# Optimization experiments

Measured on AMD Instinct MI355X. Metric: run time of the kernel, lower is better.

Reference implementation:

```python
import jax, jax.numpy as jnp
import numpy as np
from jax import lax

EPS = 1e-5
C, H, W, G = 512, 32, 32, 32


def instance_norm(x):
    # torch InstanceNorm2d: affine=False, biased variance over (H,W)
    mu = x.mean(axis=(2, 3), keepdims=True)
    var = ((x - mu) ** 2).mean(axis=(2, 3), keepdims=True)
    return (x - mu) / jnp.sqrt(var + EPS)


def conv2d(x, w, stride=1, padding=0, groups=1, lhs_dilation=None):
    return lax.conv_general_dilated(
        x, w, (stride, stride), [(padding, padding)] * 2,
        lhs_dilation=lhs_dilation, feature_group_count=groups,
        dimension_numbers=('NCHW', 'OIHW', 'NCHW'))


def leaky_relu(x):
    return jnp.where(x >= 0, x, 0.2 * x)


def unfold(img, k, s):
    # img: (C,H,W) -> (nH*nW, C, k, k); matches torch unfold(1,k,s).unfold(2,k,s)
    c, h, w = img.shape
    nH = (h - k) // s + 1
    nW = (w - k) // s + 1
    rows = []
    for i in range(k):
        cols = [img[:, i:i + s * (nH - 1) + 1:s, j:j + s * (nW - 1) + 1:s] for j in range(k)]
        rows.append(jnp.stack(cols, axis=-1))  # (C,nH,nW,k)
    p = jnp.stack(rows, axis=-2)  # (C,nH,nW,k,k)
    return p.transpose(1, 2, 0, 3, 4).reshape(nH * nW, c, k, k)


def ral(bg, fg, rate=2, ksize=3, scale=10.0):
    # Region Affinity Layer (contextual-attention style), batch = 1
    b, c, h, w = fg.shape
    fh, fw = h // rate, w // rate
    # bilinear downsample by exactly 2 (half-pixel) == 2x2 average pooling
    fg_small = fg.reshape(b, c, fh, rate, fw, rate).mean(axis=(3, 5))
    bk = 2 * rate
    bg_patches = unfold(jnp.pad(bg, ((0, 0), (0, 0), (1, 1), (1, 1)))[0], bk, rate)      # (256,C,4,4)
    fg_patches = unfold(jnp.pad(fg_small, ((0, 0), (0, 0), (1, 1), (1, 1)))[0], ksize, 1)  # (256,C,3,3)
    norm = jnp.sqrt((fg_patches ** 2).sum(axis=(1, 2, 3), keepdims=True))
    fgp_n = fg_patches / jnp.maximum(norm, 1e-4)
    score = conv2d(fg_small, fgp_n, padding=1)        # (1,256,16,16)
    attn = jax.nn.softmax(score * scale, axis=1)
    # conv_transpose2d(attn, bg_patches, stride=rate, padding=1) via lhs dilation
    w_t = jnp.flip(bg_patches, axis=(-2, -1)).transpose(1, 0, 2, 3)  # (C,256,4,4)
    return conv2d(attn, w_t, padding=bk - 2, lhs_dilation=(rate, rate)) / 4.0  # (1,C,32,32)


def forward(x, gus, w_sk3, b_sk3, w_sk5, b_sk5, w_sk7, b_sk7,
            w_fc, b_fc, w_fc0, b_fc0, w_fc1, b_fc1, w_fc2, b_fc2, w_down, w_fuse):
    # ---- SKConv (M=3 branches: k=3/5/7, groups=32) ----
    feas = []
    for wgt, bias, pad in ((w_sk3, b_sk3, 1), (w_sk5, b_sk5, 2), (w_sk7, b_sk7, 3)):
        f = conv2d(x, wgt, padding=pad, groups=G) + bias[None, :, None, None]
        feas.append(jax.nn.relu(instance_norm(f)))
    feas = jnp.stack(feas, axis=1)                # (B,3,C,H,W)
    fea_s = feas.sum(axis=1).mean(axis=(2, 3))    # (B,C) global pool
    fea_z = fea_s @ w_fc.T + b_fc                 # (B,32)
    att = jnp.stack([fea_z @ w_fc0.T + b_fc0,
                     fea_z @ w_fc1.T + b_fc1,
                     fea_z @ w_fc2.T + b_fc2], axis=1)  # (B,3,C)
    att = jax.nn.softmax(att, axis=1)[..., None, None]
    out_32 = (feas * att).sum(axis=1)             # (1,C,32,32)
    out_res = out_32
    out_32 = ral(out_32, out_32)
    b, c, h, w = out_32.shape
    # ---- gaussian-weighted broadcast sum: (P,H,W)x(C,H,W)->(P,C)->raw reshape ----
    gus_out = jnp.einsum('pxy,cxy->pc', gus, out_32[0]).reshape(b, c, h, w)
    # ---- CSA patch correlation ----
    csa2_in = jax.nn.sigmoid(out_32)
    p_fff = unfold(jnp.pad(out_32, ((0, 0), (0, 0), (1, 1), (1, 1)))[0], 3, 1)    # (1024,C,3,3)
    p_f = unfold(jnp.pad(csa2_in, ((0, 0), (0, 0), (1, 1), (1, 1)))[0], 3, 1)     # (1024,C,3,3)
    p_conv = unfold(csa2_in[0], 1, 1)                                             # (1024,C,1,1)
    csa_a = (p_conv * p_f).mean(axis=1)                                           # (1024,3,3)
    csa_a = jax.nn.softmax(csa_a.reshape(h * w, 9), axis=1).reshape(h * w, 1, 3, 3)
    out_csa = (csa_a * p_fff).sum(axis=(-2, -1)).reshape(b, c, h, w)
    # ---- fuse ----
    z = jnp.concatenate([gus_out, out_csa], axis=1)       # (1,1024,32,32)
    z = leaky_relu(instance_norm(conv2d(z, w_down)))
    z = jnp.concatenate([z, out_res], axis=1)             # (1,1024,32,32)
    return leaky_relu(instance_norm(conv2d(z, w_fuse)))   # (1,512,32,32)


def _gaussian_buffer():
    # util.gussin(1.5): gaussian centered at every grid position of a 32x32 map
    v = 1.5
    r = np.arange(32)
    i, k, x, y = np.meshgrid(r, r, r, r, indexing='ij')
    g = np.exp(-((x - i) ** 2 + (y - k) ** 2) / (2 * v * v)) / (2 * np.pi * v * v)
    return jnp.asarray(g.reshape(32 * 32, 32, 32), dtype=jnp.float32)


def setup_inputs():
    key = jax.random.key(0)
    ks = jax.random.split(key, 12)
    s = 0.02
    return {
        'x': jax.random.normal(ks[0], (1, C, H, W), jnp.float32),
        'gus': _gaussian_buffer(),
        'w_sk3': jax.random.normal(ks[1], (C, C // G, 3, 3), jnp.float32) * s,
        'b_sk3': jnp.zeros((C,), jnp.float32),
        'w_sk5': jax.random.normal(ks[2], (C, C // G, 5, 5), jnp.float32) * s,
        'b_sk5': jnp.zeros((C,), jnp.float32),
        'w_sk7': jax.random.normal(ks[3], (C, C // G, 7, 7), jnp.float32) * s,
        'b_sk7': jnp.zeros((C,), jnp.float32),
        'w_fc': jax.random.normal(ks[4], (32, C), jnp.float32) * s,
        'b_fc': jnp.zeros((32,), jnp.float32),
        'w_fc0': jax.random.normal(ks[5], (C, 32), jnp.float32) * s,
        'b_fc0': jnp.zeros((C,), jnp.float32),
        'w_fc1': jax.random.normal(ks[6], (C, 32), jnp.float32) * s,
        'b_fc1': jnp.zeros((C,), jnp.float32),
        'w_fc2': jax.random.normal(ks[7], (C, 32), jnp.float32) * s,
        'b_fc2': jnp.zeros((C,), jnp.float32),
        'w_down': jax.random.normal(ks[8], (512, 1024, 1, 1), jnp.float32) * s,
        'w_fuse': jax.random.normal(ks[9], (512, 1024, 1, 1), jnp.float32) * s,
    }


def reference(x, gus, w_sk3, b_sk3, w_sk5, b_sk5, w_sk7, b_sk7, w_fc, b_fc,
              w_fc0, b_fc0, w_fc1, b_fc1, w_fc2, b_fc2, w_down, w_fuse):
    return forward(x, gus, w_sk3, b_sk3, w_sk5, b_sk5, w_sk7, b_sk7,
                   w_fc, b_fc, w_fc0, b_fc0, w_fc1, b_fc1, w_fc2, b_fc2,
                   w_down, w_fuse)
```

## Files before the change

### kernel.cpp

```cpp
#include <hip/hip_runtime.h>
#include <math.h>

#define EPSN 1e-5f

typedef __attribute__((ext_vector_type(8))) short bf16x8;
typedef __attribute__((ext_vector_type(4))) float f32x4;

__device__ __forceinline__ ushort f2bf(float f) {
  unsigned u = __float_as_uint(f);
  unsigned r = (u + 0x7fff + ((u >> 16) & 1)) >> 16;
  return (ushort)r;
}
__device__ __forceinline__ float bf2f(ushort h) {
  return __uint_as_float(((unsigned)h) << 16);
}

__device__ __forceinline__ void breduce2(float& a, float& b, float* lds) {
#pragma unroll
  for (int o = 32; o > 0; o >>= 1) {
    a += __shfl_down(a, o);
    b += __shfl_down(b, o);
  }
  int lane = threadIdx.x & 63, wid = threadIdx.x >> 6;
  __syncthreads();
  if (lane == 0) { lds[wid] = a; lds[4 + wid] = b; }
  __syncthreads();
  a = lds[0] + lds[1] + lds[2] + lds[3];
  b = lds[4] + lds[5] + lds[6] + lds[7];
}

__device__ __forceinline__ float breduce_sum(float v, float* lds) {
#pragma unroll
  for (int o = 32; o > 0; o >>= 1) v += __shfl_down(v, o);
  int lane = threadIdx.x & 63, wid = threadIdx.x >> 6;
  __syncthreads();
  if (lane == 0) lds[wid] = v;
  __syncthreads();
  return lds[0] + lds[1] + lds[2] + lds[3];
}

__device__ __forceinline__ float breduce_max(float v, float* lds) {
#pragma unroll
  for (int o = 32; o > 0; o >>= 1) v = fmaxf(v, __shfl_down(v, o));
  int lane = threadIdx.x & 63, wid = threadIdx.x >> 6;
  __syncthreads();
  if (lane == 0) lds[wid] = v;
  __syncthreads();
  return fmaxf(fmaxf(lds[0], lds[1]), fmaxf(lds[2], lds[3]));
}

__global__ void pre_kernel(const float* __restrict__ gus,
                           const float* __restrict__ wdown,
                           const float* __restrict__ wfuse,
                           const float* __restrict__ w3,
                           const float* __restrict__ w5,
                           const float* __restrict__ w7,
                           ushort* __restrict__ gus_bf,
                           ushort* __restrict__ wdown_bf,
                           ushort* __restrict__ wfuse_bf,
                           ushort* __restrict__ resd,
                           ushort* __restrict__ Apk_g) {
  int bid = blockIdx.x, tid = threadIdx.x;
  if (bid < 2048) {
    int i = bid * 1024 + tid * 4;
    const float* src; ushort* dst; int off;
    if (i < 1048576) { src = gus; dst = gus_bf; off = i; }
    else if (i < 1572864) { src = wdown; dst = wdown_bf; off = i - 1048576; }
    else { src = wfuse; dst = wfuse_bf; off = i - 1572864; }
    float4 v = *(const float4*)&src[off];
    ushort4 o = {f2bf(v.x), f2bf(v.y), f2bf(v.z), f2bf(v.w)};
    *(ushort4*)&dst[off] = o;
  } else if (bid < 2304) {
    int t8 = (bid - 2048) * 256 + tid;
    uint4 z = {0u, 0u, 0u, 0u};
#pragma unroll
    for (int k = 0; k < 4; ++k) *(uint4*)&resd[(size_t)(t8 + k * 65536) * 8] = z;
  } else {
    int i2 = (bid - 2304) * 256 + tid;
    int g = i2 / 22016;
    int r = i2 - g * 22016;
    int p = r >> 9;
    int r5 = r & 511;
    int quad = r5 >> 7, m16 = (r5 >> 3) & 15, j = r & 7;
    int k = quad * 8 + j, tp = k >> 4, ic = k & 15;
    float val = 0.f;
    if (p < 25) {
      int t = 2 * p + tp;
      if (t < 49) val = w7[(size_t)(g * 16 + m16) * 784 + ic * 49 + t];
    } else if (p < 38) {
      int t = 2 * (p - 25) + tp;
      if (t < 25) val = w5[(size_t)(g * 16 + m16) * 400 + ic * 25 + t];
    } else {
      int t = 2 * (p - 38) + tp;
      if (t < 9) val = w3[(size_t)(g * 16 + m16) * 144 + ic * 9 + t];
    }
    Apk_g[i2] = f2bf(val);
  }
}

__global__ __launch_bounds__(256) void sk_mfma(const float* __restrict__ x,
                                               const ushort* __restrict__ Apk_g,
                                               ushort* __restrict__ feasRawH) {
  __shared__ ushort xg[10 * 38 * 24];
  int bid = blockIdx.x, tid = threadIdx.x;
  int g = bid >> 3, sl = bid & 7, y0 = sl * 4;
  for (int i = tid; i < 4560; i += 256) ((uint*)xg)[i] = 0u;
  __syncthreads();
  for (int i = tid; i < 5120; i += 256) {
    int lr = i >> 9, ic = (i >> 5) & 15, xc = i & 31;
    int y = y0 + lr - 3;
    if ((unsigned)y < 32u)
      xg[(lr * 38 + xc + 3) * 24 + ic] =
          f2bf(x[(size_t)(g * 16 + ic) * 1024 + y * 32 + xc]);
  }
  __syncthreads();
  int wv = tid >> 6, lane = tid & 63, quad = lane >> 4, m16 = lane & 15;
  int qh = (quad & 1) * 8, tp = quad >> 1;
  const ushort* Ag = Apk_g + (size_t)g * 22016;
  f32x4 acc[2][3] = {};
  for (int p = 0; p < 25; ++p) {
    bf16x8 af = *(const bf16x8*)&Ag[(p * 4 + quad) * 128 + m16 * 8];
    int t = 2 * p + tp;
    if (t > 48) t = 48;
    int ky = t / 7, kx = t - ky * 7;
#pragma unroll
    for (int ti = 0; ti < 2; ++ti) {
      int T = wv + ti * 4, tl = T >> 1, x0c = (T & 1) * 16;
      bf16x8 bf = *(const bf16x8*)&xg[((tl + ky) * 38 + x0c + m16 + kx) * 24 + qh];
      acc[ti][2] = __builtin_amdgcn_mfma_f32_16x16x32_bf16(af, bf, acc[ti][2], 0, 0, 0);
    }
  }
  for (int p = 0; p < 13; ++p) {
    bf16x8 af = *(const bf16x8*)&Ag[((p + 25) * 4 + quad) * 128 + m16 * 8];
    int t = 2 * p + tp;
    if (t > 24) t = 24;
    int ky = t / 5, kx = t - ky * 5;
#pragma unroll
    for (int ti = 0; ti < 2; ++ti) {
      int T = wv + ti * 4, tl = T >> 1, x0c = (T & 1) * 16;
      bf16x8 bf =
          *(const bf16x8*)&xg[((tl + ky + 1) * 38 + x0c + m16 + kx + 1) * 24 + qh];
      acc[ti][1] = __builtin_amdgcn_mfma_f32_16x16x32_bf16(af, bf, acc[ti][1], 0, 0, 0);
    }
  }
  for (int p = 0; p < 5; ++p) {
    bf16x8 af = *(const bf16x8*)&Ag[((p + 38) * 4 + quad) * 128 + m16 * 8];
    int t = 2 * p + tp;
    if (t > 8) t = 8;
    int ky = t / 3, kx = t - ky * 3;
#pragma unroll
    for (int ti = 0; ti < 2; ++ti) {
      int T = wv + ti * 4, tl = T >> 1, x0c = (T & 1) * 16;
      bf16x8 bf =
          *(const bf16x8*)&xg[((tl + ky + 2) * 38 + x0c + m16 + kx + 2) * 24 + qh];
      acc[ti][0] = __builtin_amdgcn_mfma_f32_16x16x32_bf16(af, bf, acc[ti][0], 0, 0, 0);
    }
  }
  int cb = g * 16 + quad * 4;
#pragma unroll
  for (int ti = 0; ti < 2; ++ti) {
    int T = wv + ti * 4, tl = T >> 1, x0c = (T & 1) * 16;
    int pos = (y0 + tl) * 32 + x0c + m16;
#pragma unroll
    for (int br = 0; br < 3; ++br)
#pragma unroll
      for (int r = 0; r < 4; ++r)
        feasRawH[(size_t)(br * 512 + cb + r) * 1024 + pos] = f2bf(acc[ti][br][r]);
  }
}

__global__ __launch_bounds__(256) void sk_norm(const ushort* __restrict__ rawH,
                                               ushort* __restrict__ feasH,
                                               float* __restrict__ bmean) {
  __shared__ float red[8];
  int mc = blockIdx.x, tid = threadIdx.x;
  float v[4];
  {
    ushort4 h = *(const ushort4*)&rawH[(size_t)mc * 1024 + tid * 4];
    v[0] = bf2f(h.x); v[1] = bf2f(h.y); v[2] = bf2f(h.z); v[3] = bf2f(h.w);
  }
  float s = 0.f, ss = 0.f;
#pragma unroll
  for (int r = 0; r < 4; ++r) { s += v[r]; ss += v[r] * v[r]; }
  breduce2(s, ss, red);
  float mean = s * (1.f / 1024.f);
  float var = ss * (1.f / 1024.f) - mean * mean;
  float inv = rsqrtf(var + EPSN);
  float rs = 0.f;
  ushort4 o;
#pragma unroll
  for (int r = 0; r < 4; ++r) {
    float t = (v[r] - mean) * inv;
    t = t > 0.f ? t : 0.f;
    ((ushort*)&o)[r] = f2bf(t);
    rs += t;
  }
  *(ushort4*)&feasH[(size_t)mc * 1024 + tid * 4] = o;
  float tot = breduce_sum(rs, red);
  if (tid == 0) bmean[mc] = tot * (1.f / 1024.f);
}

__global__ __launch_bounds__(256) void blend_fc(
    const ushort* __restrict__ feasH, const float* __restrict__ bmean,
    const float* __restrict__ wfc, const float* __restrict__ bfc,
    const float* __restrict__ w0, const float* __restrict__ b0,
    const float* __restrict__ w1, const float* __restrict__ b1,
    const float* __restrict__ w2, const float* __restrict__ b2,
    float* __restrict__ res, ushort* __restrict__ Zt2,
    ushort* __restrict__ resd) {
  __shared__ float sfea[512];
  __shared__ float zpart[8][32];
  __shared__ float zz[32];
  __shared__ float lv[3][32];
  __shared__ float attb[3][32];
  __shared__ float tile[32][33];
  int tid = threadIdx.x;
  int pb = blockIdx.x * 32, cb = blockIdx.y * 32;
  for (int c = tid; c < 512; c += 256)
    sfea[c] = bmean[c] + bmean[512 + c] + bmean[1024 + c];
  __syncthreads();
  {
    int j = tid & 31, seg = tid >> 5;
    float p = 0.f;
    for (int c = seg * 64; c < seg * 64 + 64; ++c) p += sfea[c] * wfc[j * 512 + c];
    zpart[seg][j] = p;
  }
  __syncthreads();
  if (tid < 32) {
    float d = bfc[tid];
#pragma unroll
    for (int s = 0; s < 8; ++s) d += zpart[s][tid];
    zz[tid] = d;
  }
  __syncthreads();
  if (tid < 96) {
    int m = tid >> 5, cl = tid & 31;
    const float* wm = (m == 0) ? w0 : (m == 1) ? w1 : w2;
    const float* bm = (m == 0) ? b0 : (m == 1) ? b1 : b2;
    float l = bm[cb + cl];
#pragma unroll
    for (int j = 0; j < 32; ++j) l += zz[j] * wm[(cb + cl) * 32 + j];
    lv[m][cl] = l;
  }
  __syncthreads();
  if (tid < 32) {
    float l0 = lv[0][tid], l1 = lv[1][tid], l2 = lv[2][tid];
    float mx = fmaxf(l0, fmaxf(l1, l2));
    float e0 = expf(l0 - mx), e1 = expf(l1 - mx), e2 = expf(l2 - mx);
    float inv = 1.f / (e0 + e1 + e2);
    attb[0][tid] = e0 * inv; attb[1][tid] = e1 * inv; attb[2][tid] = e2 * inv;
  }
  __syncthreads();
  int tx = tid & 31, ty = tid >> 5;
  int pos = pb + tx;
  int yy = pos >> 5, xx = pos & 31;
  int ki0 = (yy + 1) & 1, pi0 = (yy + 1 - ki0) >> 1;
  int kj0 = (xx + 1) & 1, pj0 = (xx + 1 - kj0) >> 1;
#pragma unroll
  for (int r = 0; r < 4; ++r) {
    int cl = ty + r * 8;
    int c = cb + cl;
    float v = bf2f(feasH[(size_t)c * 1024 + pos]) * attb[0][cl] +
              bf2f(feasH[(size_t)(512 + c) * 1024 + pos]) * attb[1][cl] +
              bf2f(feasH[(size_t)(1024 + c) * 1024 + pos]) * attb[2][cl];
    res[c * 1024 + pos] = v;
    tile[cl][tx] = v;
    ushort bv16 = f2bf(v);
#pragma unroll
    for (int ai = 0; ai < 2; ++ai) {
      int ki = ki0 + 2 * ai, pi = pi0 - ai;
      if ((unsigned)pi >= 16u) continue;
#pragma unroll
      for (int aj = 0; aj < 2; ++aj) {
        int kj = kj0 + 2 * aj, pj = pj0 - aj;
        if ((unsigned)pj >= 16u) continue;
        resd[((size_t)(ki * 4 + kj) << 17) + (size_t)c * 256 + pi * 16 + pj] = bv16;
      }
    }
  }
  __syncthreads();
#pragma unroll
  for (int r = 0; r < 4; ++r) {
    int pl = ty + r * 8;
    Zt2[(size_t)(pb + pl) * 1024 + 512 + cb + tx] = f2bf(tile[tx][pl]);
  }
}

__global__ __launch_bounds__(256) void gram_part2(const float* __restrict__ res,
                                                  float* __restrict__ Apart) {
  __shared__ float ch[4][324];
  int tid = threadIdx.x;
  int qb = blockIdx.x * 64, pb = blockIdx.y * 64;
  int kc = blockIdx.z;
  int tx = tid & 15, ty = tid >> 4;
  for (int i = tid; i < 4 * 324; i += 256) ((float*)ch)[i] = 0.f;
  int pi = (pb + ty * 4) >> 4, pj = (pb + ty * 4) & 15;
  int qi = (qb + tx * 4) >> 4, qj = (qb + tx * 4) & 15;
  int lane = tid & 63, wv = tid >> 6;
  int sr = lane >> 2, sc = (lane & 3) * 4;
  float acc[4][4] = {};
  for (int c0 = kc * 16; c0 < kc * 16 + 16; c0 += 4) {
    __syncthreads();
    {
      const float* src = res + (size_t)(c0 + wv) * 1024 + (2 * sr) * 32 + 2 * sc;
      float4 r0a = *(const float4*)src;
      float4 r0b = *(const float4*)(src + 4);
      float4 r1a = *(const float4*)(src + 32);
      float4 r1b = *(const float4*)(src + 36);
      float* dst = &ch[wv][(sr + 1) * 18 + sc + 1];
      dst[0] = 0.25f * (r0a.x + r0a.y + r1a.x + r1a.y);
      dst[1] = 0.25f * (r0a.z + r0a.w + r1a.z + r1a.w);
      dst[2] = 0.25f * (r0b.x + r0b.y + r1b.x + r1b.y);
      dst[3] = 0.25f * (r0b.z + r0b.w + r1b.z + r1b.w);
    }
    __syncthreads();
#pragma unroll
    for (int cc = 0; cc < 4; ++cc) {
      float ps[3][6], qs[3][6];
#pragma unroll
      for (int u = 0; u < 3; ++u) {
        const float* pr = &ch[cc][(pi + u) * 18 + pj];
        const float* qr = &ch[cc][(qi + u) * 18 + qj];
#pragma unroll
        for (int t = 0; t < 6; ++t) { ps[u][t] = pr[t]; qs[u][t] = qr[t]; }
      }
#pragma unroll
      for (int u = 0; u < 3; ++u)
#pragma unroll
        for (int v = 0; v < 3; ++v)
#pragma unroll
          for (int i = 0; i < 4; ++i)
#pragma unroll
            for (int j = 0; j < 4; ++j)
              acc[i][j] += ps[u][v + i] * qs[u][v + j];
    }
  }
#pragma unroll
  for (int i = 0; i < 4; ++i) {
    float4 o4 = {acc[i][0], acc[i][1], acc[i][2], acc[i][3]};
    *(float4*)&Apart[(size_t)kc * 65536 + (pb + ty * 4 + i) * 256 + qb + tx * 4] = o4;
  }
}

__global__ __launch_bounds__(256) void attn_soft3(const float* __restrict__ Apart,
                                                  ushort* __restrict__ attnT) {
  __shared__ float red[8];
  int q = blockIdx.x, t = threadIdx.x;
  float d = 0.f, s = 0.f;
#pragma unroll
  for (int k = 0; k < 32; ++k) {
    d += Apart[(size_t)k * 65536 + t * 257];
    s += Apart[(size_t)k * 65536 + q * 256 + t];
  }
  float invn = 10.f / fmaxf(sqrtf(fmaxf(d, 0.f)), 1e-4f);
  float v = s * invn;
  float mx = breduce_max(v, red);
  float e = expf(v - mx);
  float sm = breduce_sum(e, red);
  attnT[q * 256 + t] = f2bf(e / sm);
}

__global__ __launch_bounds__(256) void mfma_tconv(const ushort* __restrict__ attnT,
                                                  const ushort* __restrict__ resd,
                                                  float* __restrict__ T) {
  int tid = threadIdx.x;
  int wv = tid >> 6, lane = tid & 63;
  int quad = lane >> 4, m16 = lane & 15;
  int nb = blockIdx.x * 64, qb = blockIdx.y * 64;
  int b = blockIdx.z;
  const ushort* Ap = attnT + (size_t)(qb + wv * 16 + m16) * 256 + quad * 8;
  const ushort* Bp = resd + (size_t)b * 131072 + (size_t)(nb + m16) * 256 + quad * 8;
  f32x4 ac0 = {0.f, 0.f, 0.f, 0.f}, ac1 = ac0, ac2 = ac0, ac3 = ac0;
#pragma unroll 2
  for (int k0 = 0; k0 < 256; k0 += 32) {
    bf16x8 af = *(const bf16x8*)(Ap + k0);
    bf16x8 b0 = *(const bf16x8*)(Bp + k0);
    bf16x8 b1 = *(const bf16x8*)(Bp + 16 * 256 + k0);
    bf16x8 b2 = *(const bf16x8*)(Bp + 32 * 256 + k0);
    bf16x8 b3 = *(const bf16x8*)(Bp + 48 * 256 + k0);
    ac0 = __builtin_amdgcn_mfma_f32_16x16x32_bf16(af, b0, ac0, 0, 0, 0);
    ac1 = __builtin_amdgcn_mfma_f32_16x16x32_bf16(af, b1, ac1, 0, 0, 0);
    ac2 = __builtin_amdgcn_mfma_f32_16x16x32_bf16(af, b2, ac2, 0, 0, 0);
    ac3 = __builtin_amdgcn_mfma_f32_16x16x32_bf16(af, b3, ac3, 0, 0, 0);
  }
  int row = qb + wv * 16 + quad * 4;
  float* Cb = T + (size_t)b * 131072;
  f32x4 accs[4] = {ac0, ac1, ac2, ac3};
#pragma unroll
  for (int nt = 0; nt < 4; ++nt)
#pragma unroll
    for (int r = 0; r < 4; ++r)
      Cb[(size_t)(row + r) * 512 + nb + nt * 16 + m16] = accs[nt][r];
}

__global__ __launch_bounds__(256) void tcomb2(const float* __restrict__ T,
                                              float* __restrict__ orlt,
                                              float* __restrict__ sigt,
                                              ushort* __restrict__ orlT) {
  __shared__ float tl[32][33];
  int nb = blockIdx.x * 32, cb = blockIdx.y * 32;
  int tx = threadIdx.x & 31, ty = threadIdx.x >> 5;
#pragma unroll
  for (int r = 0; r < 4; ++r) {
    int nl = ty + r * 8;
    int n = nb + nl, c = cb + tx;
    int y = n >> 5, x = n & 31;
    int i0 = (y + 1) >> 1, ki0 = (y + 1) & 1;
    int j0 = (x + 1) >> 1, kj0 = (x + 1) & 1;
    float sum = 0.f;
#pragma unroll
    for (int iy = 0; iy < 2; ++iy) {
      int i = i0 - iy, ki = ki0 + 2 * iy;
      if ((unsigned)i >= 16u) continue;
#pragma unroll
      for (int ix = 0; ix < 2; ++ix) {
        int j = j0 - ix, kj = kj0 + 2 * ix;
        if ((unsigned)j >= 16u) continue;
        sum += T[((ki * 4 + kj) * 256 + i * 16 + j) * 512 + c];
      }
    }
    float v = sum * 0.25f;
    orlt[n * 512 + c] = v;
    sigt[n * 512 + c] = 1.f / (1.f + expf(-v));
    tl[nl][tx] = v;
  }
  __syncthreads();
#pragma unroll
  for (int r = 0; r < 4; ++r) {
    int cl = ty + r * 8;
    orlT[(size_t)(cb + cl) * 1024 + nb + tx] = f2bf(tl[tx][cl]);
  }
}

__global__ __launch_bounds__(256) void gus_csa(
    const ushort* __restrict__ gus_bf, const ushort* __restrict__ orlT,
    const float* __restrict__ sigt, const float* __restrict__ orlt,
    ushort* __restrict__ Zt) {
  __shared__ float red9[4][9];
  __shared__ float a9s[9];
  int tid = threadIdx.x;
  if (blockIdx.x < 128) {
    const int K = 1024;
    int wv = tid >> 6, lane = tid & 63;
    int quad = lane >> 4, m16 = lane & 15;
    int nb = (blockIdx.x & 7) * 64, mb = (blockIdx.x >> 3) * 64;
    const ushort* Ap = gus_bf + (size_t)(mb + wv * 16 + m16) * K + quad * 8;
    const ushort* Bp = orlT + (size_t)(nb + m16) * K + quad * 8;
    f32x4 ac0 = {0.f, 0.f, 0.f, 0.f}, ac1 = ac0, ac2 = ac0, ac3 = ac0;
#pragma unroll 2
    for (int k0 = 0; k0 < K; k0 += 32) {
      bf16x8 af = *(const bf16x8*)(Ap + k0);
      bf16x8 b0 = *(const bf16x8*)(Bp + k0);
      bf16x8 b1 = *(const bf16x8*)(Bp + (size_t)16 * K + k0);
      bf16x8 b2 = *(const bf16x8*)(Bp + (size_t)32 * K + k0);
      bf16x8 b3 = *(const bf16x8*)(Bp + (size_t)48 * K + k0);
      ac0 = __builtin_amdgcn_mfma_f32_16x16x32_bf16(af, b0, ac0, 0, 0, 0);
      ac1 = __builtin_amdgcn_mfma_f32_16x16x32_bf16(af, b1, ac1, 0, 0, 0);
      ac2 = __builtin_amdgcn_mfma_f32_16x16x32_bf16(af, b2, ac2, 0, 0, 0);
      ac3 = __builtin_amdgcn_mfma_f32_16x16x32_bf16(af, b3, ac3, 0, 0, 0);
    }
    int row = mb + wv * 16 + quad * 4;
    f32x4 accs[4] = {ac0, ac1, ac2, ac3};
#pragma unroll
    for (int nt = 0; nt < 4; ++nt) {
      int c = nb + nt * 16 + m16;
#pragma unroll
      for (int r = 0; r < 4; ++r) {
        int p = row + r;
        int pos = ((p & 1) << 9) + c;
        int kk = p >> 1;
        Zt[(size_t)pos * 1024 + kk] = f2bf(accs[nt][r]);
      }
    }
    return;
  }
  int n = blockIdx.x - 128;
  int ny = n >> 5, nx = n & 31;
  int c2 = tid * 2;
  int lane = tid & 63, wid = tid >> 6;
  float2 ctr = *(const float2*)&sigt[n * 512 + c2];
  float part[9];
#pragma unroll
  for (int u = 0; u < 3; ++u) {
    int yy = ny + u - 1;
#pragma unroll
    for (int v = 0; v < 3; ++v) {
      int xx = nx + v - 1;
      float2 nb2 = {0.f, 0.f};
      if ((unsigned)yy < 32u && (unsigned)xx < 32u)
        nb2 = *(const float2*)&sigt[(yy * 32 + xx) * 512 + c2];
      part[u * 3 + v] = ctr.x * nb2.x + ctr.y * nb2.y;
    }
  }
#pragma unroll
  for (int t = 0; t < 9; ++t)
#pragma unroll
    for (int o = 32; o > 0; o >>= 1) part[t] += __shfl_down(part[t], o);
  if (lane == 0)
#pragma unroll
    for (int t = 0; t < 9; ++t) red9[wid][t] = part[t];
  __syncthreads();
  if (tid == 0) {
    float a[9];
#pragma unroll
    for (int t = 0; t < 9; ++t)
      a[t] = (red9[0][t] + red9[1][t] + red9[2][t] + red9[3][t]) * (1.f / 512.f);
    float mx = a[0];
#pragma unroll
    for (int t = 1; t < 9; ++t) mx = fmaxf(mx, a[t]);
    float sum = 0.f;
#pragma unroll
    for (int t = 0; t < 9; ++t) { a[t] = expf(a[t] - mx); sum += a[t]; }
    float inv = 1.f / sum;
#pragma unroll
    for (int t = 0; t < 9; ++t) a9s[t] = a[t] * inv;
  }
  __syncthreads();
  float2 acc = {0.f, 0.f};
#pragma unroll
  for (int u = 0; u < 3; ++u) {
    int yy = ny + u - 1;
#pragma unroll
    for (int v = 0; v < 3; ++v) {
      int xx = nx + v - 1;
      if ((unsigned)yy < 32u && (unsigned)xx < 32u) {
        float w = a9s[u * 3 + v];
        float2 ov = *(const float2*)&orlt[(yy * 32 + xx) * 512 + c2];
        acc.x += w * ov.x;
        acc.y += w * ov.y;
      }
    }
  }
  int kk = 512 + (n >> 1);
  int pos0 = ((n & 1) << 9) + c2;
  Zt[(size_t)pos0 * 1024 + kk] = f2bf(acc.x);
  Zt[(size_t)(pos0 + 1) * 1024 + kk] = f2bf(acc.y);
}

__global__ __launch_bounds__(256) void mfma_gemm_ks(const ushort* __restrict__ A,
                                                    const ushort* __restrict__ Bt,
                                                    float* __restrict__ Cp,
                                                    int N) {
  const int KF = 1024;
  int tid = threadIdx.x;
  int wv = tid >> 6, lane = tid & 63;
  int quad = lane >> 4, m16 = lane & 15;
  int nb = blockIdx.x * 64, mb = blockIdx.y * 64;
  int kh = blockIdx.z;
  const ushort* Ap = A + (size_t)(mb + wv * 16 + m16) * KF + kh * 512 + quad * 8;
  const ushort* Bp = Bt + (size_t)(nb + m16) * KF + kh * 512 + quad * 8;
  f32x4 ac0 = {0.f, 0.f, 0.f, 0.f}, ac1 = ac0, ac2 = ac0, ac3 = ac0;
#pragma unroll 2
  for (int k0 = 0; k0 < 512; k0 += 32) {
    bf16x8 af = *(const bf16x8*)(Ap + k0);
    bf16x8 b0 = *(const bf16x8*)(Bp + k0);
    bf16x8 b1 = *(const bf16x8*)(Bp + (size_t)16 * KF + k0);
    bf16x8 b2 = *(const bf16x8*)(Bp + (size_t)32 * KF + k0);
    bf16x8 b3 = *(const bf16x8*)(Bp + (size_t)48 * KF + k0);
    ac0 = __builtin_amdgcn_mfma_f32_16x16x32_bf16(af, b0, ac0, 0, 0, 0);
    ac1 = __builtin_amdgcn_mfma_f32_16x16x32_bf16(af, b1, ac1, 0, 0, 0);
    ac2 = __builtin_amdgcn_mfma_f32_16x16x32_bf16(af, b2, ac2, 0, 0, 0);
    ac3 = __builtin_amdgcn_mfma_f32_16x16x32_bf16(af, b3, ac3, 0, 0, 0);
  }
  int row = mb + wv * 16 + quad * 4;
  float* C = Cp + (size_t)kh * 524288;
  f32x4 accs[4] = {ac0, ac1, ac2, ac3};
#pragma unroll
  for (int nt = 0; nt < 4; ++nt)
#pragma unroll
    for (int r = 0; r < 4; ++r)
      C[(size_t)(row + r) * N + nb + nt * 16 + m16] = accs[nt][r];
}

__global__ __launch_bounds__(256) void norm_down2(const float* __restrict__ ra,
                                                  ushort* __restrict__ Zt2) {
  __shared__ float red[8];
  int c = blockIdx.x, tid = threadIdx.x;
  float v[4];
  float s = 0.f, ss = 0.f;
#pragma unroll
  for (int r = 0; r < 4; ++r) {
    int i = c * 1024 + tid + r * 256;
    v[r] = ra[i] + ra[524288 + i];
    s += v[r];
    ss += v[r] * v[r];
  }
  breduce2(s, ss, red);
  float mean = s * (1.f / 1024.f);
  float var = ss * (1.f / 1024.f) - mean * mean;
  float inv = rsqrtf(var + EPSN);
#pragma unroll
  for (int r = 0; r < 4; ++r) {
    float t = (v[r] - mean) * inv;
    t = t >= 0.f ? t : 0.2f * t;
    Zt2[(size_t)(tid + r * 256) * 1024 + c] = f2bf(t);
  }
}

__global__ __launch_bounds__(256) void norm_leaky2(const float* __restrict__ ra,
                                                   float* __restrict__ out) {
  __shared__ float red[8];
  int c = blockIdx.x, tid = threadIdx.x;
  float v[4];
  float s = 0.f, ss = 0.f;
#pragma unroll
  for (int r = 0; r < 4; ++r) {
    int i = c * 1024 + tid + r * 256;
    v[r] = ra[i] + ra[524288 + i];
    s += v[r];
    ss += v[r] * v[r];
  }
  breduce2(s, ss, red);
  float mean = s * (1.f / 1024.f);
  float var = ss * (1.f / 1024.f) - mean * mean;
  float inv = rsqrtf(var + EPSN);
#pragma unroll
  for (int r = 0; r < 4; ++r) {
    float t = (v[r] - mean) * inv;
    out[c * 1024 + tid + r * 256] = t >= 0.f ? t : 0.2f * t;
  }
}

extern "C" void kernel_launch(void* const* d_in, const int* in_sizes, int n_in,
                              void* d_out, int out_size, void* d_ws, size_t ws_size,
                              hipStream_t stream) {
  const float* x = (const float*)d_in[0];
  const float* gus = (const float*)d_in[1];
  const float* w3 = (const float*)d_in[2];
  const float* w5 = (const float*)d_in[4];
  const float* w7 = (const float*)d_in[6];
  const float* wfc = (const float*)d_in[8];
  const float* bfc = (const float*)d_in[9];
  const float* w0 = (const float*)d_in[10];
  const float* b0 = (const float*)d_in[11];
  const float* w1 = (const float*)d_in[12];
  const float* b1 = (const float*)d_in[13];
  const float* w2 = (const float*)d_in[14];
  const float* b2 = (const float*)d_in[15];
  const float* wdown = (const float*)d_in[16];
  const float* wfuse = (const float*)d_in[17];

  float* ws = (float*)d_ws;
  ushort* feasH = (ushort*)ws;
  float* rawP = ws + 786432;
  float* bmean = ws + 1835008;
  float* res = bmean + 1536;
  float* Zt2f = res + 524288;
  ushort* Zt2 = (ushort*)Zt2f;
  float* T = Zt2f + 524288;
  ushort* feasRawH = (ushort*)T;
  float* Apart = T;
  ushort* Zt = (ushort*)T;
  float* orlt = T + 2097152;
  float* sigt = orlt + 524288;
  ushort* orlT = (ushort*)(sigt + 524288);
  ushort* attnT = (ushort*)(sigt + 786432);
  ushort* gus_bf = (ushort*)(sigt + 819200);
  ushort* wdown_bf = (ushort*)(sigt + 1343488);
  ushort* wfuse_bf = (ushort*)(sigt + 1605632);
  ushort* resd = (ushort*)(sigt + 1867776);
  ushort* Apk_g = (ushort*)(sigt + 2916352);

  pre_kernel<<<5056, 256, 0, stream>>>(gus, wdown, wfuse, w3, w5, w7, gus_bf,
                                       wdown_bf, wfuse_bf, resd, Apk_g);
  sk_mfma<<<256, 256, 0, stream>>>(x, Apk_g, feasRawH);
  sk_norm<<<1536, 256, 0, stream>>>(feasRawH, feasH, bmean);
  blend_fc<<<dim3(32, 16), 256, 0, stream>>>(feasH, bmean, wfc, bfc, w0, b0, w1,
                                             b1, w2, b2, res, Zt2, resd);
  gram_part2<<<dim3(4, 4, 32), 256, 0, stream>>>(res, Apart);
  attn_soft3<<<256, 256, 0, stream>>>(Apart, attnT);
  mfma_tconv<<<dim3(8, 4, 16), 256, 0, stream>>>(attnT, resd, T);
  tcomb2<<<dim3(32, 16), 256, 0, stream>>>(T, orlt, sigt, orlT);
  gus_csa<<<1152, 256, 0, stream>>>(gus_bf, orlT, sigt, orlt, Zt);
  mfma_gemm_ks<<<dim3(16, 8, 2), 256, 0, stream>>>(wdown_bf, Zt, rawP, 1024);
  norm_down2<<<512, 256, 0, stream>>>(rawP, Zt2);
  mfma_gemm_ks<<<dim3(16, 8, 2), 256, 0, stream>>>(wfuse_bf, Zt2, rawP, 1024);
  norm_leaky2<<<512, 256, 0, stream>>>(rawP, (float*)d_out);
}
```

Before: 239.5 us.

## Fold transposed-conv tap combination into a single parity-class GEMM

```diff
diff --git a/kernel.cpp b/kernel.cpp
--- a/kernel.cpp
+++ b/kernel.cpp
@@ -59,23 +59,35 @@
                            ushort* __restrict__ wdown_bf,
                            ushort* __restrict__ wfuse_bf,
                            ushort* __restrict__ resd,
-                           ushort* __restrict__ Apk_g) {
+                           ushort* __restrict__ Apk_g,
+                           ushort* __restrict__ Acomb) {
   int bid = blockIdx.x, tid = threadIdx.x;
   if (bid < 2048) {
     int i = bid * 1024 + tid * 4;
-    const float* src; ushort* dst; int off;
-    if (i < 1048576) { src = gus; dst = gus_bf; off = i; }
-    else if (i < 1572864) { src = wdown; dst = wdown_bf; off = i - 1048576; }
-    else { src = wfuse; dst = wfuse_bf; off = i - 1572864; }
-    float4 v = *(const float4*)&src[off];
-    ushort4 o = {f2bf(v.x), f2bf(v.y), f2bf(v.z), f2bf(v.w)};
-    *(ushort4*)&dst[off] = o;
+    if (i < 1048576) {
+      float4 v = *(const float4*)&gus[i];
+      int m = i >> 10, n = i & 1023;
+      int y = n >> 5, x = n & 31;
+      int idxb = ((y >> 1) << 4) + (x >> 1);
+      int py = y & 1;
+      ushort2 e0 = {f2bf(v.x), f2bf(v.z)};
+      ushort2 e1 = {f2bf(v.y), f2bf(v.w)};
+      *(ushort2*)&gus_bf[(size_t)m * 1024 + (py * 2 + 0) * 256 + idxb] = e0;
+      *(ushort2*)&gus_bf[(size_t)m * 1024 + (py * 2 + 1) * 256 + idxb] = e1;
+    } else {
+      const float* src; ushort* dst; int off;
+      if (i < 1572864) { src = wdown; dst = wdown_bf; off = i - 1048576; }
+      else { src = wfuse; dst = wfuse_bf; off = i - 1572864; }
+      float4 v = *(const float4*)&src[off];
+      ushort4 o = {f2bf(v.x), f2bf(v.y), f2bf(v.z), f2bf(v.w)};
+      *(ushort4*)&dst[off] = o;
+    }
   } else if (bid < 2304) {
     int t8 = (bid - 2048) * 256 + tid;
     uint4 z = {0u, 0u, 0u, 0u};
 #pragma unroll
     for (int k = 0; k < 4; ++k) *(uint4*)&resd[(size_t)(t8 + k * 65536) * 8] = z;
-  } else {
+  } else if (bid < 5056) {
     int i2 = (bid - 2304) * 256 + tid;
     int g = i2 / 22016;
     int r = i2 - g * 22016;
@@ -95,6 +107,10 @@
       if (t < 9) val = w3[(size_t)(g * 16 + m16) * 144 + ic * 9 + t];
     }
     Apk_g[i2] = f2bf(val);
+  } else {
+    int j = (bid - 5056) * 256 + tid;
+    uint4 z = {0u, 0u, 0u, 0u};
+    ((uint4*)Acomb)[j] = z;
   }
 }
 
@@ -342,8 +358,8 @@
   }
 }
 
-__global__ __launch_bounds__(256) void attn_soft3(const float* __restrict__ Apart,
-                                                  ushort* __restrict__ attnT) {
+__global__ __launch_bounds__(256) void attn_soft4(const float* __restrict__ Apart,
+                                                  ushort* __restrict__ Acomb) {
   __shared__ float red[8];
   int q = blockIdx.x, t = threadIdx.x;
   float d = 0.f, s = 0.f;
@@ -357,78 +373,79 @@
   float mx = breduce_max(v, red);
   float e = expf(v - mx);
   float sm = breduce_sum(e, red);
-  attnT[q * 256 + t] = f2bf(e / sm);
-}
-
-__global__ __launch_bounds__(256) void mfma_tconv(const ushort* __restrict__ attnT,
-                                                  const ushort* __restrict__ resd,
-                                                  float* __restrict__ T) {
-  int tid = threadIdx.x;
-  int wv = tid >> 6, lane = tid & 63;
-  int quad = lane >> 4, m16 = lane & 15;
-  int nb = blockIdx.x * 64, qb = blockIdx.y * 64;
-  int b = blockIdx.z;
-  const ushort* Ap = attnT + (size_t)(qb + wv * 16 + m16) * 256 + quad * 8;
-  const ushort* Bp = resd + (size_t)b * 131072 + (size_t)(nb + m16) * 256 + quad * 8;
-  f32x4 ac0 = {0.f, 0.f, 0.f, 0.f}, ac1 = ac0, ac2 = ac0, ac3 = ac0;
-#pragma unroll 2
-  for (int k0 = 0; k0 < 256; k0 += 32) {
-    bf16x8 af = *(const bf16x8*)(Ap + k0);
-    bf16x8 b0 = *(const bf16x8*)(Bp + k0);
-    bf16x8 b1 = *(const bf16x8*)(Bp + 16 * 256 + k0);
-    bf16x8 b2 = *(const bf16x8*)(Bp + 32 * 256 + k0);
-    bf16x8 b3 = *(const bf16x8*)(Bp + 48 * 256 + k0);
-    ac0 = __builtin_amdgcn_mfma_f32_16x16x32_bf16(af, b0, ac0, 0, 0, 0);
-    ac1 = __builtin_amdgcn_mfma_f32_16x16x32_bf16(af, b1, ac1, 0, 0, 0);
-    ac2 = __builtin_amdgcn_mfma_f32_16x16x32_bf16(af, b2, ac2, 0, 0, 0);
-    ac3 = __builtin_amdgcn_mfma_f32_16x16x32_bf16(af, b3, ac3, 0, 0, 0);
-  }
-  int row = qb + wv * 16 + quad * 4;
-  float* Cb = T + (size_t)b * 131072;
-  f32x4 accs[4] = {ac0, ac1, ac2, ac3};
-#pragma unroll
-  for (int nt = 0; nt < 4; ++nt)
-#pragma unroll
-    for (int r = 0; r < 4; ++r)
-      Cb[(size_t)(row + r) * 512 + nb + nt * 16 + m16] = accs[nt][r];
-}
-
-__global__ __launch_bounds__(256) void tcomb2(const float* __restrict__ T,
+  ushort val = f2bf(e / sm);
+  int qi = q >> 4, qj = q & 15;
+#pragma unroll
+  for (int ki = 0; ki < 4; ++ki) {
+    int y = 2 * qi + ki - 1;
+    if ((unsigned)y >= 32u) continue;
+#pragma unroll
+    for (int kj = 0; kj < 4; ++kj) {
+      int x = 2 * qj + kj - 1;
+      if ((unsigned)x >= 32u) continue;
+      int cls = (y & 1) * 2 + (x & 1);
+      int idx = ((y >> 1) << 4) + (x >> 1);
+      int seg = ((ki >> 1) << 1) + (kj >> 1);
+      Acomb[(size_t)(cls * 256 + idx) * 1024 + seg * 256 + t] = val;
+    }
+  }
+}
+
+__global__ __launch_bounds__(256) void tconv2(const ushort* __restrict__ Acomb,
+                                              const ushort* __restrict__ resd,
                                               float* __restrict__ orlt,
                                               float* __restrict__ sigt,
                                               ushort* __restrict__ orlT) {
-  __shared__ float tl[32][33];
-  int nb = blockIdx.x * 32, cb = blockIdx.y * 32;
-  int tx = threadIdx.x & 31, ty = threadIdx.x >> 5;
-#pragma unroll
-  for (int r = 0; r < 4; ++r) {
-    int nl = ty + r * 8;
-    int n = nb + nl, c = cb + tx;
-    int y = n >> 5, x = n & 31;
-    int i0 = (y + 1) >> 1, ki0 = (y + 1) & 1;
-    int j0 = (x + 1) >> 1, kj0 = (x + 1) & 1;
-    float sum = 0.f;
-#pragma unroll
-    for (int iy = 0; iy < 2; ++iy) {
-      int i = i0 - iy, ki = ki0 + 2 * iy;
-      if ((unsigned)i >= 16u) continue;
-#pragma unroll
-      for (int ix = 0; ix < 2; ++ix) {
-        int j = j0 - ix, kj = kj0 + 2 * ix;
-        if ((unsigned)j >= 16u) continue;
-        sum += T[((ki * 4 + kj) * 256 + i * 16 + j) * 512 + c];
-      }
-    }
-    float v = sum * 0.25f;
-    orlt[n * 512 + c] = v;
-    sigt[n * 512 + c] = 1.f / (1.f + expf(-v));
-    tl[nl][tx] = v;
-  }
-  __syncthreads();
-#pragma unroll
-  for (int r = 0; r < 4; ++r) {
-    int cl = ty + r * 8;
-    orlT[(size_t)(cb + cl) * 1024 + nb + tx] = f2bf(tl[tx][cl]);
+  __shared__ float tl[64][33];
+  int tid = threadIdx.x;
+  int wv = tid >> 6, lane = tid & 63, quad = lane >> 4, m16 = lane & 15;
+  int nb = blockIdx.x * 32;
+  int mb = blockIdx.y * 64;
+  int cls = blockIdx.y >> 2;
+  int py = cls >> 1, px = cls & 1;
+  int row0 = mb + wv * 16 + m16;
+  const ushort* Ap = Acomb + (size_t)row0 * 1024 + quad * 8;
+  f32x4 ac0 = {0.f, 0.f, 0.f, 0.f}, ac1 = ac0;
+#pragma unroll
+  for (int sg = 0; sg < 4; ++sg) {
+    int ki = 2 * (sg >> 1) + 1 - py;
+    int kj = 2 * (sg & 1) + 1 - px;
+    const ushort* Bp =
+        resd + ((size_t)(ki * 4 + kj) << 17) + (size_t)(nb + m16) * 256 + quad * 8;
+    const ushort* As = Ap + sg * 256;
+#pragma unroll 2
+    for (int k0 = 0; k0 < 256; k0 += 32) {
+      bf16x8 af = *(const bf16x8*)(As + k0);
+      bf16x8 b0 = *(const bf16x8*)(Bp + k0);
+      bf16x8 b1 = *(const bf16x8*)(Bp + 16 * 256 + k0);
+      ac0 = __builtin_amdgcn_mfma_f32_16x16x32_bf16(af, b0, ac0, 0, 0, 0);
+      ac1 = __builtin_amdgcn_mfma_f32_16x16x32_bf16(af, b1, ac1, 0, 0, 0);
+    }
+  }
+  int rloc0 = wv * 16 + quad * 4;
+  f32x4 accs[2] = {ac0, ac1};
+#pragma unroll
+  for (int nt = 0; nt < 2; ++nt) {
+    int c = nb + nt * 16 + m16;
+#pragma unroll
+    for (int r = 0; r < 4; ++r) {
+      int rl = rloc0 + r;
+      int idx = (mb + rl) & 255;
+      int y = ((idx >> 4) << 1) + py;
+      int x = ((idx & 15) << 1) + px;
+      int n = y * 32 + x;
+      float v = accs[nt][r] * 0.25f;
+      orlt[n * 512 + c] = v;
+      sigt[n * 512 + c] = 1.f / (1.f + expf(-v));
+      tl[rl][nt * 16 + m16] = v;
+    }
+  }
+  __syncthreads();
+  int r_l = tid & 63;
+#pragma unroll
+  for (int k = 0; k < 8; ++k) {
+    int c_l = (tid >> 6) + k * 4;
+    orlT[(size_t)(nb + c_l) * 1024 + mb + r_l] = f2bf(tl[r_l][c_l]);
   }
 }
 
@@ -643,6 +660,7 @@
   float* ws = (float*)d_ws;
   ushort* feasH = (ushort*)ws;
   float* rawP = ws + 786432;
+  ushort* Acomb = (ushort*)rawP;
   float* bmean = ws + 1835008;
   float* res = bmean + 1536;
   float* Zt2f = res + 524288;
@@ -654,23 +672,21 @@
   float* orlt = T + 2097152;
   float* sigt = orlt + 524288;
   ushort* orlT = (ushort*)(sigt + 524288);
-  ushort* attnT = (ushort*)(sigt + 786432);
   ushort* gus_bf = (ushort*)(sigt + 819200);
   ushort* wdown_bf = (ushort*)(sigt + 1343488);
   ushort* wfuse_bf = (ushort*)(sigt + 1605632);
   ushort* resd = (ushort*)(sigt + 1867776);
   ushort* Apk_g = (ushort*)(sigt + 2916352);
 
-  pre_kernel<<<5056, 256, 0, stream>>>(gus, wdown, wfuse, w3, w5, w7, gus_bf,
-                                       wdown_bf, wfuse_bf, resd, Apk_g);
+  pre_kernel<<<5568, 256, 0, stream>>>(gus, wdown, wfuse, w3, w5, w7, gus_bf,
+                                       wdown_bf, wfuse_bf, resd, Apk_g, Acomb);
   sk_mfma<<<256, 256, 0, stream>>>(x, Apk_g, feasRawH);
   sk_norm<<<1536, 256, 0, stream>>>(feasRawH, feasH, bmean);
   blend_fc<<<dim3(32, 16), 256, 0, stream>>>(feasH, bmean, wfc, bfc, w0, b0, w1,
                                              b1, w2, b2, res, Zt2, resd);
   gram_part2<<<dim3(4, 4, 32), 256, 0, stream>>>(res, Apart);
-  attn_soft3<<<256, 256, 0, stream>>>(Apart, attnT);
-  mfma_tconv<<<dim3(8, 4, 16), 256, 0, stream>>>(attnT, resd, T);
-  tcomb2<<<dim3(32, 16), 256, 0, stream>>>(T, orlt, sigt, orlT);
+  attn_soft4<<<256, 256, 0, stream>>>(Apart, Acomb);
+  tconv2<<<dim3(16, 16), 256, 0, stream>>>(Acomb, resd, orlt, sigt, orlT);
   gus_csa<<<1152, 256, 0, stream>>>(gus_bf, orlT, sigt, orlt, Zt);
   mfma_gemm_ks<<<dim3(16, 8, 2), 256, 0, stream>>>(wdown_bf, Zt, rawP, 1024);
   norm_down2<<<512, 256, 0, stream>>>(rawP, Zt2);
```

New measurement: 232.8 us. -2.8%, faster.
